# Kernel optimization log

Measured on AMD Instinct MI355X. Metric: run time of the kernel, lower is better.

Reference implementation:

```python
import jax, jax.numpy as jnp
import numpy as np

# Static configuration (values of input_spatial_shapes are compile-time constants,
# mirroring how Deformable DETR fixes the FPN level sizes per image resolution).
SPATIAL_SHAPES = [(128, 128), (64, 64), (32, 32), (16, 16)]
N_HEADS = 8
N_LEVELS = 4
N_POINTS = 4
D_MODEL = 256
HEAD_DIM = D_MODEL // N_HEADS  # 32


def setup_inputs() -> dict:
    key = jax.random.key(0)
    ks = jax.random.split(key, 12)
    n = 1
    len_in = sum(h * w for h, w in SPATIAL_SHAPES)  # 21760
    len_q = len_in
    s = 0.02
    inp = {
        "query": jax.random.normal(ks[0], (n, len_q, D_MODEL), jnp.float32),
        "reference_points": jax.random.uniform(ks[1], (n, len_q, N_LEVELS, 2), jnp.float32),
        "input_flatten": jax.random.normal(ks[2], (n, len_in, D_MODEL), jnp.float32),
        "input_spatial_shapes": jnp.array(SPATIAL_SHAPES, jnp.int32),
        "input_level_start_index": jnp.array(
            np.cumsum([0] + [h * w for h, w in SPATIAL_SHAPES[:-1]]), jnp.int32
        ),
        # learned parameters (nn.Linear stores weight as [out, in])
        "W_off": jax.random.normal(ks[3], (N_HEADS * N_LEVELS * N_POINTS * 2, D_MODEL), jnp.float32) * s,
        "b_off": jax.random.normal(ks[4], (N_HEADS * N_LEVELS * N_POINTS * 2,), jnp.float32) * 0.5,
        "W_attn": jax.random.normal(ks[5], (N_HEADS * N_LEVELS * N_POINTS, D_MODEL), jnp.float32) * s,
        "b_attn": jnp.zeros((N_HEADS * N_LEVELS * N_POINTS,), jnp.float32),
        "W_val": jax.random.normal(ks[6], (D_MODEL, D_MODEL), jnp.float32) * s,
        "b_val": jnp.zeros((D_MODEL,), jnp.float32),
        "W_out": jax.random.normal(ks[7], (D_MODEL, D_MODEL), jnp.float32) * s,
        "b_out": jnp.zeros((D_MODEL,), jnp.float32),
    }
    return inp


def _bilinear_sample(img, grid, h, w):
    """torch F.grid_sample(mode='bilinear', padding_mode='zeros', align_corners=False).
    img:  [B, C, h, w]; grid: [B, Q, P, 2] in [-1, 1] -> returns [B, C, Q, P]."""
    B, C = img.shape[0], img.shape[1]
    Q, P = grid.shape[1], grid.shape[2]
    gx = (grid[..., 0] + 1.0) * (w * 0.5) - 0.5
    gy = (grid[..., 1] + 1.0) * (h * 0.5) - 0.5
    x0 = jnp.floor(gx)
    y0 = jnp.floor(gy)
    lx, ly = gx - x0, gy - y0
    x0i = x0.astype(jnp.int32)
    y0i = y0.astype(jnp.int32)
    flat = img.reshape(B, C, h * w)
    acc = jnp.zeros((B, C, Q * P), img.dtype)
    for dx, dy, wgt in (
        (0, 0, (1 - lx) * (1 - ly)),
        (1, 0, lx * (1 - ly)),
        (0, 1, (1 - lx) * ly),
        (1, 1, lx * ly),
    ):
        xi = x0i + dx
        yi = y0i + dy
        valid = (xi >= 0) & (xi < w) & (yi >= 0) & (yi < h)
        idx = (jnp.clip(yi, 0, h - 1) * w + jnp.clip(xi, 0, w - 1)).reshape(B, Q * P)
        vals = jnp.take_along_axis(flat, jnp.broadcast_to(idx[:, None, :], (B, C, Q * P)), axis=2)
        acc = acc + vals * (wgt * valid.astype(img.dtype)).reshape(B, 1, Q * P)
    return acc.reshape(B, C, Q, P)


def reference(query, reference_points, input_flatten, input_spatial_shapes,
              input_level_start_index, W_off, b_off, W_attn, b_attn,
              W_val, b_val, W_out, b_out):
    n, Q, C = query.shape
    # value projection
    value = input_flatten @ W_val.T + b_val                      # [n, Lin, C]
    value = value.reshape(n, -1, N_HEADS, HEAD_DIM)              # [n, Lin, H, D]
    # sampling offsets & attention weights from query
    off = (query @ W_off.T + b_off).reshape(n, Q, N_HEADS, N_LEVELS, N_POINTS, 2)
    aw = jax.nn.softmax(
        (query @ W_attn.T + b_attn).reshape(n, Q, N_HEADS, N_LEVELS * N_POINTS), axis=-1
    ).reshape(n, Q, N_HEADS, N_LEVELS, N_POINTS)
    # reference_points has last dim 2: normalize offsets by (w, h) per level
    norm = jnp.array([[w, h] for h, w in SPATIAL_SHAPES], jnp.float32)  # [L, 2]
    loc = reference_points[:, :, None, :, None, :] + off / norm[None, None, None, :, None, :]
    grids = 2.0 * loc - 1.0                                       # [n,Q,H,L,P,2]
    aw_t = aw.transpose(0, 2, 1, 3, 4).reshape(n * N_HEADS, 1, Q, N_LEVELS, N_POINTS)
    out = jnp.zeros((n * N_HEADS, HEAD_DIM, Q), query.dtype)
    start = 0
    for lvl, (h, w) in enumerate(SPATIAL_SHAPES):
        v = value[:, start:start + h * w]                         # [n, hw, H, D]
        start += h * w
        img = v.transpose(0, 2, 3, 1).reshape(n * N_HEADS, HEAD_DIM, h, w)
        g = grids[:, :, :, lvl].transpose(0, 2, 1, 3, 4).reshape(n * N_HEADS, Q, N_POINTS, 2)
        sampled = _bilinear_sample(img, g, h, w)                  # [nH, D, Q, P]
        out = out + (sampled * aw_t[:, :, :, lvl, :]).sum(-1)
    out = out.reshape(n, N_HEADS * HEAD_DIM, Q).transpose(0, 2, 1)  # [n, Q, C]
    return out @ W_out.T + b_out
```

## Files before the change

### kernel.cpp

```cpp
#include <hip/hip_runtime.h>
#include <math.h>

#define Q_TOTAL 21760
#define NBLK_M 340
#define QB 8

typedef short        s16x8 __attribute__((ext_vector_type(8)));
typedef __bf16       bfv8  __attribute__((ext_vector_type(8)));
typedef float        f32x4 __attribute__((ext_vector_type(4)));
typedef unsigned int u32x4 __attribute__((ext_vector_type(4)));

__device__ __forceinline__ s16x8 pack8(float4 a, float4 b) {
    bfv8 t;
    t[0] = (__bf16)a.x; t[1] = (__bf16)a.y; t[2] = (__bf16)a.z; t[3] = (__bf16)a.w;
    t[4] = (__bf16)b.x; t[5] = (__bf16)b.y; t[6] = (__bf16)b.z; t[7] = (__bf16)b.w;
    return __builtin_bit_cast(s16x8, t);
}

__global__ __launch_bounds__(256) void cvt_weights(
    const float* __restrict__ Woff, const float* __restrict__ Wattn,
    const float* __restrict__ Wval, const float* __restrict__ Wout,
    const float* __restrict__ boff, const float* __restrict__ battn,
    unsigned short* __restrict__ dst, float* __restrict__ bias_cat)
{
    if (blockIdx.x == 224) {
        const int t = threadIdx.x;
        bias_cat[t] = boff[t];
        if (t < 128) bias_cat[256 + t] = battn[t];
        return;
    }
    const int e = blockIdx.x * 1024 + threadIdx.x * 4;
    const float* src; int base;
    if (e < 65536)       { src = Woff;  base = 0; }
    else if (e < 98304)  { src = Wattn; base = 65536; }
    else if (e < 163840) { src = Wval;  base = 98304; }
    else                 { src = Wout;  base = 163840; }
    float4 v = *(const float4*)(src + (e - base));
    ushort4 o;
    o.x = __builtin_bit_cast(unsigned short, (__bf16)v.x);
    o.y = __builtin_bit_cast(unsigned short, (__bf16)v.y);
    o.z = __builtin_bit_cast(unsigned short, (__bf16)v.z);
    o.w = __builtin_bit_cast(unsigned short, (__bf16)v.w);
    *(ushort4*)(dst + e) = o;
}

template<int BN, bool A_BF16, bool C_BF16>
__global__ __launch_bounds__(256) void gemm_mfma(
    const void* __restrict__ Avoid,
    const unsigned short* __restrict__ W16,
    const float* __restrict__ bias,
    void* __restrict__ Cvoid,
    int ldc)
{
    constexpr int K = 256, BM = 64;
    constexpr int NB2 = BN / 2;
    constexpr int NF = NB2 / 16;
    __shared__ unsigned short As[BM * 32];
    __shared__ unsigned short Bs[BN * 32];

    const int tid  = threadIdx.x;
    const int lane = tid & 63;
    const int wv   = tid >> 6;
    const int wr   = wv >> 1, wc = wv & 1;
    const int rowBase = blockIdx.x * BM;

    const int sr    = tid >> 2;
    const int skq   = (tid & 3) * 8;
    const int sslot = (tid & 3) * 16;

    f32x4 acc[2][NF];
#pragma unroll
    for (int i = 0; i < 2; i++)
#pragma unroll
        for (int j = 0; j < NF; j++) acc[i][j] = (f32x4){0.f, 0.f, 0.f, 0.f};

    const size_t arow = (size_t)(rowBase + sr) * K;

    for (int kt = 0; kt < K; kt += 32) {
        s16x8 aval;
        if constexpr (A_BF16) {
            const unsigned short* A16 = (const unsigned short*)Avoid;
            aval = *(const s16x8*)(A16 + arow + kt + skq);
        } else {
            const float* A32 = (const float*)Avoid;
            const float* p = A32 + arow + kt + skq;
            aval = pack8(*(const float4*)p, *(const float4*)(p + 4));
        }
        s16x8 bval[BN / 64];
#pragma unroll
        for (int c = 0; c < BN / 64; c++) {
            const unsigned short* p = W16 + (size_t)(c * 64 + sr) * K + kt + skq;
            bval[c] = *(const s16x8*)p;
        }
        __syncthreads();
        *(s16x8*)(As + (((sr * 64 + sslot) ^ ((sr & 7) << 4)) >> 1)) = aval;
#pragma unroll
        for (int c = 0; c < BN / 64; c++) {
            const int row = c * 64 + sr;
            *(s16x8*)(Bs + (((row * 64 + sslot) ^ ((row & 7) << 4)) >> 1)) = bval[c];
        }
        __syncthreads();
        s16x8 af[2];
#pragma unroll
        for (int mi = 0; mi < 2; mi++) {
            const int row = wr * 32 + mi * 16 + (lane & 15);
            af[mi] = *(const s16x8*)(As + (((row * 64 + (lane >> 4) * 16) ^ ((row & 7) << 4)) >> 1));
        }
#pragma unroll
        for (int ni = 0; ni < NF; ni++) {
            const int row = wc * NB2 + ni * 16 + (lane & 15);
            s16x8 bfrag = *(const s16x8*)(Bs + (((row * 64 + (lane >> 4) * 16) ^ ((row & 7) << 4)) >> 1));
#pragma unroll
            for (int mi = 0; mi < 2; mi++)
                acc[mi][ni] = __builtin_amdgcn_mfma_f32_16x16x32_bf16(af[mi], bfrag, acc[mi][ni], 0, 0, 0);
        }
    }

#pragma unroll
    for (int ni = 0; ni < NF; ni++) {
        const int col = wc * NB2 + ni * 16 + (lane & 15);
        const float bv = bias[col];
#pragma unroll
        for (int mi = 0; mi < 2; mi++) {
            const int r0 = rowBase + wr * 32 + mi * 16 + (lane >> 4) * 4;
#pragma unroll
            for (int j = 0; j < 4; j++) {
                const float v = acc[mi][ni][j] + bv;
                if constexpr (C_BF16) {
                    ((unsigned short*)Cvoid)[(size_t)(r0 + j) * ldc + col] =
                        __builtin_bit_cast(unsigned short, (__bf16)v);
                } else {
                    ((float*)Cvoid)[(size_t)(r0 + j) * ldc + col] = v;
                }
            }
        }
    }
}

__global__ __launch_bounds__(256) void sample_kernel(
    const unsigned short* __restrict__ value,
    const float* __restrict__ offattn,
    const float* __restrict__ refpts,
    unsigned short* __restrict__ sampled)
{
    __shared__ int2 s_iw[64 * 65];

    const int tid   = threadIdx.x;
    const int qbase = blockIdx.x * QB;

    {
        const int g  = tid >> 2;
        const int l  = tid & 3;
        const int ql = g >> 3, h = g & 7;
        const int q  = qbase + ql;
        const float* oa = offattn + (size_t)q * 384;

        float4 lg = *(const float4*)(oa + 256 + h * 16 + l * 4);
        float m = fmaxf(fmaxf(lg.x, lg.y), fmaxf(lg.z, lg.w));
        m = fmaxf(m, __shfl_xor(m, 1));
        m = fmaxf(m, __shfl_xor(m, 2));
        float e0 = __expf(lg.x - m), e1 = __expf(lg.y - m),
              e2 = __expf(lg.z - m), e3 = __expf(lg.w - m);
        float s = e0 + e1 + e2 + e3;
        s += __shfl_xor(s, 1);
        s += __shfl_xor(s, 2);
        const float inv = 1.f / s;
        float aw[4] = {e0 * inv, e1 * inv, e2 * inv, e3 * inv};

        const float4 o01 = *(const float4*)(oa + h * 32 + l * 8);
        const float4 o23 = *(const float4*)(oa + h * 32 + l * 8 + 4);
        const float2 rp  = *(const float2*)(refpts + (size_t)q * 8 + l * 2);
        const int   SZ[4] = {128, 64, 32, 16};
        const int   ST[4] = {0, 16384, 20480, 21504};
        const float S = (float)SZ[l];
        const int   W_ = SZ[l], START = ST[l];
        const float oxs[4] = {o01.x, o01.z, o23.x, o23.z};
        const float oys[4] = {o01.y, o01.w, o23.y, o23.w};
        int2* dst = &s_iw[g * 65 + l * 16];
#pragma unroll
        for (int p = 0; p < 4; p++) {
            const float gx = (rp.x + oxs[p] / S) * S - 0.5f;
            const float gy = (rp.y + oys[p] / S) * S - 0.5f;
            const float x0f = floorf(gx), y0f = floorf(gy);
            const float lx = gx - x0f, ly = gy - y0f;
            const int x0 = (int)x0f, y0 = (int)y0f;
            const float a = aw[p];
#pragma unroll
            for (int tap = 0; tap < 4; tap++) {
                const int dx = tap & 1, dy = tap >> 1;
                const int xi = x0 + dx, yi = y0 + dy;
                const bool valid = (xi >= 0) & (xi < W_) & (yi >= 0) & (yi < W_);
                const float wx = dx ? lx : 1.f - lx;
                const float wy = dy ? ly : 1.f - ly;
                int2 r;
                r.x = valid ? (START + yi * W_ + xi) : 0;
                r.y = __float_as_int(valid ? wx * wy * a : 0.f);
                dst[p * 4 + tap] = r;
            }
        }
    }
    __syncthreads();

    {
        const int d8 = tid & 3;
        const int h  = (tid >> 2) & 7;
        const int ql = tid >> 5;
        const int q  = qbase + ql;
        const int g  = ql * 8 + h;
        const int2* iw = &s_iw[g * 65];
        const char* vb = (const char*)value + (h * 64 + d8 * 16);

        float acc[8] = {0.f, 0.f, 0.f, 0.f, 0.f, 0.f, 0.f, 0.f};
#pragma unroll 8
        for (int i = 0; i < 64; i++) {
            const int2 p = iw[i];
            const float w = __int_as_float(p.y);
            const u32x4 uv = *(const u32x4*)(vb + (size_t)(unsigned)p.x * 512);
#pragma unroll
            for (int r = 0; r < 4; r++) {
                const float lo = __uint_as_float(uv[r] << 16);
                const float hi = __uint_as_float(uv[r] & 0xffff0000u);
                acc[2 * r]     = fmaf(lo, w, acc[2 * r]);
                acc[2 * r + 1] = fmaf(hi, w, acc[2 * r + 1]);
            }
        }
        s16x8 o = pack8(make_float4(acc[0], acc[1], acc[2], acc[3]),
                        make_float4(acc[4], acc[5], acc[6], acc[7]));
        *(s16x8*)(sampled + (size_t)q * 256 + h * 32 + d8 * 8) = o;
    }
}

extern "C" void kernel_launch(void* const* d_in, const int* in_sizes, int n_in,
                              void* d_out, int out_size, void* d_ws, size_t ws_size,
                              hipStream_t stream) {
    const float* query  = (const float*)d_in[0];
    const float* refpts = (const float*)d_in[1];
    const float* input_flatten = (const float*)d_in[2];
    const float* W_off  = (const float*)d_in[5];
    const float* b_off  = (const float*)d_in[6];
    const float* W_attn = (const float*)d_in[7];
    const float* b_attn = (const float*)d_in[8];
    const float* W_val  = (const float*)d_in[9];
    const float* b_val  = (const float*)d_in[10];
    const float* W_out  = (const float*)d_in[11];
    const float* b_out  = (const float*)d_in[12];
    float* out = (float*)d_out;

    char* ws = (char*)d_ws;
    unsigned short* value   = (unsigned short*)ws;
    float*          offattn = (float*)(ws + 11141120);
    unsigned short* sampled = (unsigned short*)(ws + 44564480);
    unsigned short* w16     = (unsigned short*)(ws + 55705600);
    float*          bias_cat= (float*)(ws + 56164352);
    unsigned short* w16_val  = w16 + 98304;
    unsigned short* w16_out  = w16 + 163840;

    cvt_weights<<<225, 256, 0, stream>>>(W_off, W_attn, W_val, W_out, b_off, b_attn, w16, bias_cat);

    gemm_mfma<256, false, true ><<<NBLK_M, 256, 0, stream>>>(input_flatten, w16_val, b_val, value, 256);
    gemm_mfma<384, false, false><<<NBLK_M, 256, 0, stream>>>(query, w16, bias_cat, offattn, 384);
    sample_kernel<<<Q_TOTAL / QB, 256, 0, stream>>>(value, offattn, refpts, sampled);
    gemm_mfma<256, true,  false><<<NBLK_M, 256, 0, stream>>>(sampled, w16_out, b_out, out, 256);
}
```

Baseline: 98.77 us.

## Split GEMM columns across grid and pack sample index/weight into 32 bits

The GEMMs now use a fixed 128-column tile with a 2D grid, so more blocks run with fewer accumulators per thread. The cost is that the A tile is reloaded once per column block. The sampling kernel packs the 16-bit sample index and a bf16 weight into one 32-bit LDS word, halving LDS traffic and footprint. The price is lower precision for the bilinear-times-attention weight, and the index must fit in 16 bits (21760 does fit).

New measurement: 95.90 us. 1.03x faster.

```diff
diff --git a/kernel.cpp b/kernel.cpp
--- a/kernel.cpp
+++ b/kernel.cpp
@@ -44,7 +44,7 @@
     *(ushort4*)(dst + e) = o;
 }
 
-template<int BN, bool A_BF16, bool C_BF16>
+template<bool A_BF16, bool C_BF16>
 __global__ __launch_bounds__(256) void gemm_mfma(
     const void* __restrict__ Avoid,
     const unsigned short* __restrict__ W16,
@@ -52,7 +52,7 @@
     void* __restrict__ Cvoid,
     int ldc)
 {
-    constexpr int K = 256, BM = 64;
+    constexpr int K = 256, BM = 64, BN = 128;
     constexpr int NB2 = BN / 2;
     constexpr int NF = NB2 / 16;
     __shared__ unsigned short As[BM * 32];
@@ -63,6 +63,7 @@
     const int wv   = tid >> 6;
     const int wr   = wv >> 1, wc = wv & 1;
     const int rowBase = blockIdx.x * BM;
+    const int colBase = blockIdx.y * BN;
 
     const int sr    = tid >> 2;
     const int skq   = (tid & 3) * 8;
@@ -86,16 +87,16 @@
             const float* p = A32 + arow + kt + skq;
             aval = pack8(*(const float4*)p, *(const float4*)(p + 4));
         }
-        s16x8 bval[BN / 64];
-#pragma unroll
-        for (int c = 0; c < BN / 64; c++) {
-            const unsigned short* p = W16 + (size_t)(c * 64 + sr) * K + kt + skq;
+        s16x8 bval[2];
+#pragma unroll
+        for (int c = 0; c < 2; c++) {
+            const unsigned short* p = W16 + (size_t)(colBase + c * 64 + sr) * K + kt + skq;
             bval[c] = *(const s16x8*)p;
         }
         __syncthreads();
         *(s16x8*)(As + (((sr * 64 + sslot) ^ ((sr & 7) << 4)) >> 1)) = aval;
 #pragma unroll
-        for (int c = 0; c < BN / 64; c++) {
+        for (int c = 0; c < 2; c++) {
             const int row = c * 64 + sr;
             *(s16x8*)(Bs + (((row * 64 + sslot) ^ ((row & 7) << 4)) >> 1)) = bval[c];
         }
@@ -118,7 +119,7 @@
 
 #pragma unroll
     for (int ni = 0; ni < NF; ni++) {
-        const int col = wc * NB2 + ni * 16 + (lane & 15);
+        const int col = colBase + wc * NB2 + ni * 16 + (lane & 15);
         const float bv = bias[col];
 #pragma unroll
         for (int mi = 0; mi < 2; mi++) {
@@ -143,7 +144,7 @@
     const float* __restrict__ refpts,
     unsigned short* __restrict__ sampled)
 {
-    __shared__ int2 s_iw[64 * 65];
+    __shared__ unsigned s_iw[64 * 65];
 
     const int tid   = threadIdx.x;
     const int qbase = blockIdx.x * QB;
@@ -176,7 +177,7 @@
         const int   W_ = SZ[l], START = ST[l];
         const float oxs[4] = {o01.x, o01.z, o23.x, o23.z};
         const float oys[4] = {o01.y, o01.w, o23.y, o23.w};
-        int2* dst = &s_iw[g * 65 + l * 16];
+        unsigned* dst = &s_iw[g * 65 + l * 16];
 #pragma unroll
         for (int p = 0; p < 4; p++) {
             const float gx = (rp.x + oxs[p] / S) * S - 0.5f;
@@ -192,10 +193,10 @@
                 const bool valid = (xi >= 0) & (xi < W_) & (yi >= 0) & (yi < W_);
                 const float wx = dx ? lx : 1.f - lx;
                 const float wy = dy ? ly : 1.f - ly;
-                int2 r;
-                r.x = valid ? (START + yi * W_ + xi) : 0;
-                r.y = __float_as_int(valid ? wx * wy * a : 0.f);
-                dst[p * 4 + tap] = r;
+                const float wgt = valid ? wx * wy * a : 0.f;
+                const unsigned idx = valid ? (unsigned)(START + yi * W_ + xi) : 0u;
+                const unsigned wb = (unsigned)__builtin_bit_cast(unsigned short, (__bf16)wgt);
+                dst[p * 4 + tap] = (idx << 16) | wb;
             }
         }
     }
@@ -207,15 +208,16 @@
         const int ql = tid >> 5;
         const int q  = qbase + ql;
         const int g  = ql * 8 + h;
-        const int2* iw = &s_iw[g * 65];
+        const unsigned* iw = &s_iw[g * 65];
         const char* vb = (const char*)value + (h * 64 + d8 * 16);
 
         float acc[8] = {0.f, 0.f, 0.f, 0.f, 0.f, 0.f, 0.f, 0.f};
 #pragma unroll 8
         for (int i = 0; i < 64; i++) {
-            const int2 p = iw[i];
-            const float w = __int_as_float(p.y);
-            const u32x4 uv = *(const u32x4*)(vb + (size_t)(unsigned)p.x * 512);
+            const unsigned u = iw[i];
+            const float w = __uint_as_float(u << 16);
+            const unsigned ofs = (u >> 16) << 9;
+            const u32x4 uv = *(const u32x4*)(vb + ofs);
 #pragma unroll
             for (int r = 0; r < 4; r++) {
                 const float lo = __uint_as_float(uv[r] << 16);
@@ -257,8 +259,8 @@
 
     cvt_weights<<<225, 256, 0, stream>>>(W_off, W_attn, W_val, W_out, b_off, b_attn, w16, bias_cat);
 
-    gemm_mfma<256, false, true ><<<NBLK_M, 256, 0, stream>>>(input_flatten, w16_val, b_val, value, 256);
-    gemm_mfma<384, false, false><<<NBLK_M, 256, 0, stream>>>(query, w16, bias_cat, offattn, 384);
+    gemm_mfma<false, true ><<<dim3(NBLK_M, 2), 256, 0, stream>>>(input_flatten, w16_val, b_val, value, 256);
+    gemm_mfma<false, false><<<dim3(NBLK_M, 3), 256, 0, stream>>>(query, w16, bias_cat, offattn, 384);
     sample_kernel<<<Q_TOTAL / QB, 256, 0, stream>>>(value, offattn, refpts, sampled);
-    gemm_mfma<256, true,  false><<<NBLK_M, 256, 0, stream>>>(sampled, w16_out, b_out, out, 256);
-}
+    gemm_mfma<true,  false><<<dim3(NBLK_M, 2), 256, 0, stream>>>(sampled, w16_out, b_out, out, 256);
+}
```
